# Kernel tuning notes

Hardware: AMD Instinct MI355X
Metric: run time of the kernel (lower is better)

## Reference

```python
import jax, jax.numpy as jnp
import numpy as np

PS = 2      # patch_size
TOPK = 3    # topk


def setup_inputs() -> dict:
    key = jax.random.key(0)
    x = jax.random.normal(key, (8, 128, 64, 64), dtype=jnp.float32)
    alpha = jnp.asarray(5.0, dtype=jnp.float32)  # nn.Parameter alpha
    return {"x": x, "alpha": alpha}


def _forward(x, alpha):
    ps = PS
    b, c, h, w = x.shape
    nph, npw = h // ps, w // ps
    npatch = nph * npw
    pa = ps * ps
    # F.normalize(p=2, dim=-3) with torch eps=1e-12
    norm = jnp.maximum(jnp.sqrt(jnp.sum(x * x, axis=1, keepdims=True)), 1e-12)
    x = x / norm
    # patchify -> [b, c, npatch, patch_area] (patches h-major, pixels row-major)
    xp = x.reshape(b, c, nph, ps, npw, ps).transpose(0, 1, 2, 4, 3, 5)
    xp = xp.reshape(b, c, npatch, pa)
    diag_idx = jnp.arange(ps) * (ps + 1)  # [0, 3] for ps=2
    # gather diagonal pixels of each patch -> [b, ps, npatch, c]
    xd = xp[:, :, :, diag_idx].transpose(0, 3, 2, 1)
    # patch correlation matmul -> [b, ps, npatch, npatch]
    corr = jnp.einsum('bpnc,bpmc->bpnm', xd, xd)
    avg = jnp.mean(corr, axis=1, keepdims=True)
    s = jnp.concatenate([corr, avg], axis=1)  # [b, ps+1, npatch, npatch]
    # ZeroWindow gaussian mask (rat_s=0.05); channel index = patch center (r,c)
    sr, sc = 0.05 * nph, 0.05 * npw
    rr = jnp.arange(nph, dtype=jnp.float32)
    cc = jnp.arange(npw, dtype=jnp.float32)
    cent_r, cent_c = jnp.meshgrid(rr, cc, indexing='ij')
    cent_r = cent_r.reshape(npatch)
    cent_c = cent_c.reshape(npatch)
    gr = jnp.exp(-(rr[None, :] - cent_r[:, None]) ** 2 / (2.0 * sr * sr))  # [npatch, nph]
    gc = jnp.exp(-(cc[None, :] - cent_c[:, None]) ** 2 / (2.0 * sc * sc))  # [npatch, npw]
    mask = (1.0 - gr[:, :, None] * gc[:, None, :]).reshape(npatch, npatch)
    s = s * mask[None, None]
    a = s * alpha
    # double (row + col) softmax
    s = jax.nn.softmax(a, axis=-1) * jax.nn.softmax(a, axis=-2)
    # expand avg channel to all patch pixels, scatter diagonal channels back
    new_x = jnp.broadcast_to(s[:, -1:], (b, pa, npatch, npatch))
    new_x = new_x.at[:, diag_idx].set(s[:, :ps])
    # un-patchify second npatch axis to spatial [b, npatch, h, w]
    y = jnp.swapaxes(new_x, 1, 3)  # [b, npatch, npatch, pa]
    y = y.reshape(b, npatch, nph, npw, ps, ps).transpose(0, 1, 2, 4, 3, 5)
    y = y.reshape(b, npatch, h, w)
    # topk over the npatch axis (dim=-3)
    vals = jax.lax.top_k(jnp.moveaxis(y, 1, -1), TOPK)[0]  # [b, h, w, k]
    return jnp.moveaxis(vals, -1, 1)  # [b, k, h, w]


def reference(x, alpha):
    return _forward(x, alpha)
```

## Files before the change

### kernel.cpp

```cpp
#include <hip/hip_runtime.h>
#include <hip/hip_bf16.h>
#include <math.h>

#define NB 8
#define NC 128
#define NH 64
#define NW 64
#define NP 1024
#define TWO_SIG2 5.12f
#define LOG2E 1.44269504089f
#define NT 6

static const size_t PSUM_OFF_B = 0;
static const size_t CAND_OFF_B = (size_t)NB * 3 * 4 * NP * 4;
static const size_t XD_OFF_B   = CAND_OFF_B + (size_t)NB * NP * 3 * 4 * NT * 4;

typedef __bf16 bf16x8 __attribute__((ext_vector_type(8)));
typedef float f32x4 __attribute__((ext_vector_type(4)));

#define INSERT3(v, A, Bq, Cq)                          \
  {                                                    \
    const float _na = fmaxf(A, (v));                   \
    const float _nb = __builtin_amdgcn_fmed3f(A, Bq, (v)); \
    Cq = __builtin_amdgcn_fmed3f(Bq, Cq, (v));         \
    A = _na;                                           \
    Bq = _nb;                                          \
  }

#define INSERT4(v, A, Bq, Cq, Dq)                      \
  {                                                    \
    const float _na = fmaxf(A, (v));                   \
    const float _nb = __builtin_amdgcn_fmed3f(A, Bq, (v)); \
    const float _nc = __builtin_amdgcn_fmed3f(Bq, Cq, (v)); \
    Dq = __builtin_amdgcn_fmed3f(Cq, Dq, (v));         \
    A = _na; Bq = _nb; Cq = _nc;                       \
  }

__device__ __forceinline__ float packf(float g, unsigned idx) {
  return __uint_as_float((__float_as_uint(g) & 0xFFFFFF00u) | idx);
}

__global__ __launch_bounds__(1024) void k1_norm(const float* __restrict__ x,
                                                __hip_bfloat16* __restrict__ xd) {
  __shared__ __align__(16) float tile[NC * 65];
  const int chunk = blockIdx.x;
  const int p = blockIdx.y;
  const int b = blockIdx.z;
  const int t = threadIdx.x;
  const int pix = t & 63;
  const int cw = t >> 6;
  const int nbase = chunk * 64;

  {
    const int n = nbase + pix;
    const int i = ((n >> 5) << 1) + p;
    const int jf = (n & 31);
    const float* xb = x + (size_t)b * NC * NH * NW + (size_t)i * NW;
    for (int cc = 0; cc < 8; ++cc) {
      const int c = (cc << 4) + cw;
      const float2 v2 = ((const float2*)(xb + (size_t)c * NH * NW))[jf];
      tile[c * 65 + pix] = (p == 0) ? v2.x : v2.y;
    }
  }
  __syncthreads();

  const int lane = t & 63;
  const int w = t >> 6;
  for (int pg = 0; pg < 4; ++pg) {
    const int pixel = (pg << 4) + w;
    const float v0 = tile[lane * 65 + pixel];
    const float v1 = tile[(lane + 64) * 65 + pixel];
    float ss = v0 * v0 + v1 * v1;
#pragma unroll
    for (int m = 32; m >= 1; m >>= 1) ss += __shfl_xor(ss, m, 64);
    const float inv = 1.0f / fmaxf(sqrtf(ss), 1e-12f);
    __hip_bfloat16* xr = xd + ((size_t)((b * 2 + p) * NP) + nbase + pixel) * NC;
    xr[lane] = __float2bfloat16(v0 * inv);
    xr[lane + 64] = __float2bfloat16(v1 * inv);
  }
}

__global__ __launch_bounds__(256) void k2_sums(const ushort* __restrict__ xd,
                                               const float* __restrict__ alpha_p,
                                               float* __restrict__ psum,
                                               float* __restrict__ cand) {
  __shared__ __align__(16) __bf16 Bs[2][64 * 136];
  __shared__ float stage[64][3][NT];
  const int t = threadIdx.x;
  const float K = (*alpha_p) * LOG2E;
  const float Cm = -(LOG2E / TWO_SIG2);

  const int cchunk = blockIdx.x;
  const int rowtile = blockIdx.y;
  const int b = blockIdx.z;
  const int i0 = rowtile << 6;
  const int jb = cchunk << 8;

  const int wave = t >> 6;
  const int lane = t & 63;
  const int lrow = lane & 15;
  const int kq = lane >> 4;

  const __bf16* X = (const __bf16*)xd;
  const __bf16* xp0 = X + ((size_t)(b * 2 + 0) * NP) * NC;
  const __bf16* xp1 = X + ((size_t)(b * 2 + 1) * NP) * NC;

  bf16x8 a0[4], a1[4];
  {
    const __bf16* pa0 = xp0 + (size_t)(i0 + wave * 16 + lrow) * NC + kq * 8;
    const __bf16* pa1 = xp1 + (size_t)(i0 + wave * 16 + lrow) * NC + kq * 8;
#pragma unroll
    for (int kc = 0; kc < 4; ++kc) {
      a0[kc] = *(const bf16x8*)(pa0 + kc * 32);
      a1[kc] = *(const bf16x8*)(pa1 + kc * 32);
    }
  }

  const int n0 = i0 + wave * 16 + kq * 4;
  const float rnf = (float)(n0 >> 5);
  const float cn0 = (float)(n0 & 31);

  float sums[3][4];
  float Lc[3][4][4];
#pragma unroll
  for (int ch = 0; ch < 3; ++ch)
#pragma unroll
    for (int reg = 0; reg < 4; ++reg) {
      sums[ch][reg] = 0.f;
#pragma unroll
      for (int q = 0; q < 4; ++q) Lc[ch][reg][q] = -3.0e38f;
    }

  for (int sc = 0; sc < 4; ++sc) {
    const int j0 = jb + (sc << 6);
    if (sc) __syncthreads();
#pragma unroll
    for (int pl = 0; pl < 2; ++pl) {
      const float4* gb = (const float4*)(xd + ((size_t)(b * 2 + pl) * NP + j0) * NC);
#pragma unroll
      for (int it = 0; it < 4; ++it) {
        const int f = (it << 8) + t;
        const int r = f >> 4, q = f & 15;
        *(float4*)(&Bs[pl][r * 136 + q * 8]) = gb[f];
      }
    }
    __syncthreads();

    f32x4 acc[2][4];
#pragma unroll
    for (int pl = 0; pl < 2; ++pl)
#pragma unroll
      for (int ct = 0; ct < 4; ++ct)
#pragma unroll
        for (int u = 0; u < 4; ++u) acc[pl][ct][u] = 0.f;

#pragma unroll
    for (int kc = 0; kc < 4; ++kc) {
      const int kk = kc * 32 + (kq << 3);
#pragma unroll
      for (int ct = 0; ct < 4; ++ct) {
        const bf16x8 b0 = *(const bf16x8*)(&Bs[0][(ct * 16 + lrow) * 136 + kk]);
        const bf16x8 b1 = *(const bf16x8*)(&Bs[1][(ct * 16 + lrow) * 136 + kk]);
        acc[0][ct] = __builtin_amdgcn_mfma_f32_16x16x32_bf16(a0[kc], b0, acc[0][ct], 0, 0, 0);
        acc[1][ct] = __builtin_amdgcn_mfma_f32_16x16x32_bf16(a1[kc], b1, acc[1][ct], 0, 0, 0);
      }
    }

#pragma unroll
    for (int ct = 0; ct < 4; ++ct) {
      const int mc = (sc << 6) + ct * 16 + lrow;
      const int m = jb + mc;
      const float rmf = (float)(m >> 5);
      const float cmf = (float)(m & 31);
      const float dr = rnf - rmf;
      const float dr2 = dr * dr;
      const unsigned mcu = (unsigned)mc;
#pragma unroll
      for (int reg = 0; reg < 4; ++reg) {
        const float dc = cn0 + (float)reg - cmf;
        const float d2 = fmaf(dc, dc, dr2);
        const float em = __builtin_amdgcn_exp2f(d2 * Cm);
        const float fm2 = fmaf(-em, K, K);
        const float g0 = fm2 * acc[0][ct][reg];
        const float g1 = fm2 * acc[1][ct][reg];
        sums[0][reg] += __builtin_amdgcn_exp2f(g0);
        sums[1][reg] += __builtin_amdgcn_exp2f(g1);
        sums[2][reg] += __builtin_amdgcn_exp2f(0.5f * (g0 + g1));
        const float p0 = packf(g0, mcu);
        const float p1 = packf(g1, mcu);
        const float p2 = packf(g0 + g1, mcu);
        INSERT4(p0, Lc[0][reg][0], Lc[0][reg][1], Lc[0][reg][2], Lc[0][reg][3]);
        INSERT4(p1, Lc[1][reg][0], Lc[1][reg][1], Lc[1][reg][2], Lc[1][reg][3]);
        INSERT4(p2, Lc[2][reg][0], Lc[2][reg][1], Lc[2][reg][2], Lc[2][reg][3]);
      }
    }
  }

#pragma unroll
  for (int off = 1; off < 16; off <<= 1)
#pragma unroll
    for (int ch = 0; ch < 3; ++ch)
#pragma unroll
      for (int reg = 0; reg < 4; ++reg)
        sums[ch][reg] += __shfl_xor(sums[ch][reg], off, 64);

  if (lrow == 0) {
#pragma unroll
    for (int ch = 0; ch < 3; ++ch)
#pragma unroll
      for (int reg = 0; reg < 4; ++reg) {
        const int n = i0 + wave * 16 + kq * 4 + reg;
        psum[(((size_t)b * 3 + ch) * 4 + cchunk) * NP + n] = sums[ch][reg];
      }
  }

#pragma unroll
  for (int ch = 0; ch < 3; ++ch)
#pragma unroll
    for (int reg = 0; reg < 4; ++reg) {
      float l0 = Lc[ch][reg][0], l1 = Lc[ch][reg][1];
      float l2 = Lc[ch][reg][2], l3 = Lc[ch][reg][3];
      const int np = wave * 16 + kq * 4 + reg;
#pragma unroll
      for (int r = 0; r < NT; ++r) {
        float mx = l0;
        mx = fmaxf(mx, __shfl_xor(mx, 1, 64));
        mx = fmaxf(mx, __shfl_xor(mx, 2, 64));
        mx = fmaxf(mx, __shfl_xor(mx, 4, 64));
        mx = fmaxf(mx, __shfl_xor(mx, 8, 64));
        if (lrow == 0) stage[np][ch][r] = mx;
        const bool own = (l0 == mx);
        l0 = own ? l1 : l0;
        l1 = own ? l2 : l1;
        l2 = own ? l3 : l2;
        l3 = own ? -3.0e38f : l3;
      }
    }
  __syncthreads();

  for (int u = t; u < 64 * 3 * NT; u += 256) {
    const int np = u / (3 * NT);
    const int rem = u - np * (3 * NT);
    const int ch = rem / NT;
    const int r = rem - ch * NT;
    cand[(((size_t)b * NP + i0 + np) * 3 + ch) * (4 * NT) + cchunk * NT + r] =
        stage[np][ch][r];
  }
}

__global__ __launch_bounds__(256) void k5_final(const float* __restrict__ cand,
                                                const float* __restrict__ psum,
                                                float* __restrict__ out) {
  __shared__ float nlR[3][NP];
  const int t = threadIdx.x;
  const int tau = blockIdx.x * 256 + t;
  const int b = tau >> 10;
  const int n = tau & (NP - 1);

#pragma unroll
  for (int ch = 0; ch < 3; ++ch)
#pragma unroll
    for (int k = 0; k < 4; ++k) {
      const int m = (k << 8) + t;
      const float* pp = psum + ((size_t)b * 3 + ch) * 4 * NP + m;
      nlR[ch][m] = -__builtin_amdgcn_logf(pp[0] + pp[NP] + pp[2 * NP] + pp[3 * NP]);
    }
  __syncthreads();

  float irn[3];
#pragma unroll
  for (int ch = 0; ch < 3; ++ch) {
    const float* pp = psum + ((size_t)b * 3 + ch) * 4 * NP + n;
    irn[ch] = 1.0f / (pp[0] + pp[NP] + pp[2 * NP] + pp[3 * NP]);
  }

  float o0[3], o1[3], o2[3];
#pragma unroll
  for (int ch = 0; ch < 3; ++ch) {
    float tA = -3.0e38f, tB = -3.0e38f, tC = -3.0e38f;
    const float cf = (ch == 2) ? 1.0f : 2.0f;
    const float* cp = cand + (((size_t)b * NP + n) * 3 + ch) * (4 * NT);
#pragma unroll
    for (int cc = 0; cc < 4; ++cc)
#pragma unroll
      for (int r = 0; r < NT; ++r) {
        const float p = cp[cc * NT + r];
        const int mi = (cc << 8) | (int)(__float_as_uint(p) & 255u);
        const float tv = fmaf(cf, p, nlR[ch][mi]);
        INSERT3(tv, tA, tB, tC);
      }
    o0[ch] = __builtin_amdgcn_exp2f(tA) * irn[ch];
    o1[ch] = __builtin_amdgcn_exp2f(tB) * irn[ch];
    o2[ch] = __builtin_amdgcn_exp2f(tC) * irn[ch];
  }

  const int rn = n >> 5, cn = n & 31;
  float* ob = out + (size_t)b * 3 * (NH * NW);
  const int i00 = ((rn << 1) * NW) + (cn << 1);
#pragma unroll
  for (int tt = 0; tt < 3; ++tt) {
    float* op = ob + (size_t)tt * (NH * NW);
    const float r0 = (tt == 0) ? o0[0] : (tt == 1) ? o1[0] : o2[0];
    const float r1 = (tt == 0) ? o0[1] : (tt == 1) ? o1[1] : o2[1];
    const float r2 = (tt == 0) ? o0[2] : (tt == 1) ? o1[2] : o2[2];
    op[i00] = r0;
    op[i00 + NW + 1] = r1;
    op[i00 + 1] = r2;
    op[i00 + NW] = r2;
  }
}

extern "C" void kernel_launch(void* const* d_in, const int* in_sizes, int n_in,
                              void* d_out, int out_size, void* d_ws, size_t ws_size,
                              hipStream_t stream) {
  const float* x = (const float*)d_in[0];
  const float* alpha = (const float*)d_in[1];
  float* out = (float*)d_out;
  char* ws = (char*)d_ws;

  float* psum = (float*)(ws + PSUM_OFF_B);
  float* cand = (float*)(ws + CAND_OFF_B);
  __hip_bfloat16* xd = (__hip_bfloat16*)(ws + XD_OFF_B);

  k1_norm<<<dim3(16, 2, NB), 1024, 0, stream>>>(x, xd);
  k2_sums<<<dim3(4, 16, NB), 256, 0, stream>>>((const ushort*)xd, alpha, psum, cand);
  k5_final<<<dim3(32), 256, 0, stream>>>(cand, psum, out);
}
```

Before: 103.3 us.

## Double-buffer B tiles via async global_load_lds with XOR-swizzled LDS layout

After: 114.4 us. 10.8% more time.

```diff
diff --git a/kernel.cpp b/kernel.cpp
--- a/kernel.cpp
+++ b/kernel.cpp
@@ -84,7 +84,7 @@
                                                const float* __restrict__ alpha_p,
                                                float* __restrict__ psum,
                                                float* __restrict__ cand) {
-  __shared__ __align__(16) __bf16 Bs[2][64 * 136];
+  __shared__ __align__(16) __bf16 Bs[2][2][64 * 128];
   __shared__ float stage[64][3][NT];
   const int t = threadIdx.x;
   const float K = (*alpha_p) * LOG2E;
@@ -116,6 +116,25 @@
     }
   }
 
+  const int srow_l = lane >> 4;
+  const int sslot = lane & 15;
+
+#define ISSUE_TILE(buf, j0v)                                                   \
+  {                                                                            \
+    _Pragma("unroll")                                                          \
+    for (int pl = 0; pl < 2; ++pl) {                                           \
+      const ushort* gsrc = xd + ((size_t)(b * 2 + pl) * NP + (j0v)) * NC;      \
+      _Pragma("unroll")                                                        \
+      for (int it2 = 0; it2 < 4; ++it2) {                                      \
+        const int git = wave * 4 + it2;                \
+        const int row = git * 4 + srow_l;                           \
+        const int qlog = sslot ^ (row & 7);                                    \
+        const ushort* src = gsrc + (size_t)row * NC + qlog * 8;                \
+        __builtin_amdgcn_global_load_lds(src, &Bs[buf][pl][git * 512], 16, 0, 0); \
+      }                                                                        \
+    }                                                                          \
+  }
+
   const int n0 = i0 + wave * 16 + kq * 4;
   const float rnf = (float)(n0 >> 5);
   const float cn0 = (float)(n0 & 31);
@@ -131,20 +150,15 @@
       for (int q = 0; q < 4; ++q) Lc[ch][reg][q] = -3.0e38f;
     }
 
+  ISSUE_TILE(0, jb);
+  __syncthreads();
+
+#pragma unroll
   for (int sc = 0; sc < 4; ++sc) {
+    const int cur = sc & 1;
     const int j0 = jb + (sc << 6);
-    if (sc) __syncthreads();
-#pragma unroll
-    for (int pl = 0; pl < 2; ++pl) {
-      const float4* gb = (const float4*)(xd + ((size_t)(b * 2 + pl) * NP + j0) * NC);
-#pragma unroll
-      for (int it = 0; it < 4; ++it) {
-        const int f = (it << 8) + t;
-        const int r = f >> 4, q = f & 15;
-        *(float4*)(&Bs[pl][r * 136 + q * 8]) = gb[f];
-      }
-    }
-    __syncthreads();
+
+    if (sc < 3) ISSUE_TILE(cur ^ 1, jb + ((sc + 1) << 6));
 
     f32x4 acc[2][4];
 #pragma unroll
@@ -156,11 +170,13 @@
 
 #pragma unroll
     for (int kc = 0; kc < 4; ++kc) {
-      const int kk = kc * 32 + (kq << 3);
 #pragma unroll
       for (int ct = 0; ct < 4; ++ct) {
-        const bf16x8 b0 = *(const bf16x8*)(&Bs[0][(ct * 16 + lrow) * 136 + kk]);
-        const bf16x8 b1 = *(const bf16x8*)(&Bs[1][(ct * 16 + lrow) * 136 + kk]);
+        const int row = ct * 16 + lrow;
+        const int s = kc * 4 + kq;
+        const int off = row * 128 + ((s ^ (lrow & 7)) << 3);
+        const bf16x8 b0 = *(const bf16x8*)(&Bs[cur][0][off]);
+        const bf16x8 b1 = *(const bf16x8*)(&Bs[cur][1][off]);
         acc[0][ct] = __builtin_amdgcn_mfma_f32_16x16x32_bf16(a0[kc], b0, acc[0][ct], 0, 0, 0);
         acc[1][ct] = __builtin_amdgcn_mfma_f32_16x16x32_bf16(a1[kc], b1, acc[1][ct], 0, 0, 0);
       }
@@ -194,6 +210,8 @@
         INSERT4(p2, Lc[2][reg][0], Lc[2][reg][1], Lc[2][reg][2], Lc[2][reg][3]);
       }
     }
+
+    __syncthreads();
   }
 
 #pragma unroll
@@ -246,6 +264,7 @@
     cand[(((size_t)b * NP + i0 + np) * 3 + ch) * (4 * NT) + cchunk * NT + r] =
         stage[np][ch][r];
   }
+#undef ISSUE_TILE
 }
 
 __global__ __launch_bounds__(256) void k5_final(const float* __restrict__ cand,
```

## Split k2 column tiles across two wave groups with 512-thread blocks

Applied to the files above, without the earlier changes.

New measurement: 114.1 us. +10.5%, slower.

```diff
diff --git a/kernel.cpp b/kernel.cpp
--- a/kernel.cpp
+++ b/kernel.cpp
@@ -10,10 +10,11 @@
 #define TWO_SIG2 5.12f
 #define LOG2E 1.44269504089f
 #define NT 6
+#define NHALF 8
 
 static const size_t PSUM_OFF_B = 0;
-static const size_t CAND_OFF_B = (size_t)NB * 3 * 4 * NP * 4;
-static const size_t XD_OFF_B   = CAND_OFF_B + (size_t)NB * NP * 3 * 4 * NT * 4;
+static const size_t CAND_OFF_B = (size_t)NB * 3 * NHALF * NP * 4;
+static const size_t XD_OFF_B   = CAND_OFF_B + (size_t)NB * NP * 3 * NHALF * NT * 4;
 
 typedef __bf16 bf16x8 __attribute__((ext_vector_type(8)));
 typedef float f32x4 __attribute__((ext_vector_type(4)));
@@ -80,12 +81,12 @@
   }
 }
 
-__global__ __launch_bounds__(256) void k2_sums(const ushort* __restrict__ xd,
-                                               const float* __restrict__ alpha_p,
-                                               float* __restrict__ psum,
-                                               float* __restrict__ cand) {
+__global__ __launch_bounds__(512, 4) void k2_sums(const ushort* __restrict__ xd,
+                                                  const float* __restrict__ alpha_p,
+                                                  float* __restrict__ psum,
+                                                  float* __restrict__ cand) {
   __shared__ __align__(16) __bf16 Bs[2][64 * 136];
-  __shared__ float stage[64][3][NT];
+  __shared__ float stage[64][3][2][NT];
   const int t = threadIdx.x;
   const float K = (*alpha_p) * LOG2E;
   const float Cm = -(LOG2E / TWO_SIG2);
@@ -100,6 +101,8 @@
   const int lane = t & 63;
   const int lrow = lane & 15;
   const int kq = lane >> 4;
+  const int wg = wave >> 2;
+  const int wr = wave & 3;
 
   const __bf16* X = (const __bf16*)xd;
   const __bf16* xp0 = X + ((size_t)(b * 2 + 0) * NP) * NC;
@@ -107,8 +110,8 @@
 
   bf16x8 a0[4], a1[4];
   {
-    const __bf16* pa0 = xp0 + (size_t)(i0 + wave * 16 + lrow) * NC + kq * 8;
-    const __bf16* pa1 = xp1 + (size_t)(i0 + wave * 16 + lrow) * NC + kq * 8;
+    const __bf16* pa0 = xp0 + (size_t)(i0 + wr * 16 + lrow) * NC + kq * 8;
+    const __bf16* pa1 = xp1 + (size_t)(i0 + wr * 16 + lrow) * NC + kq * 8;
 #pragma unroll
     for (int kc = 0; kc < 4; ++kc) {
       a0[kc] = *(const bf16x8*)(pa0 + kc * 32);
@@ -116,7 +119,7 @@
     }
   }
 
-  const int n0 = i0 + wave * 16 + kq * 4;
+  const int n0 = i0 + wr * 16 + kq * 4;
   const float rnf = (float)(n0 >> 5);
   const float cn0 = (float)(n0 & 31);
 
@@ -138,36 +141,38 @@
     for (int pl = 0; pl < 2; ++pl) {
       const float4* gb = (const float4*)(xd + ((size_t)(b * 2 + pl) * NP + j0) * NC);
 #pragma unroll
-      for (int it = 0; it < 4; ++it) {
-        const int f = (it << 8) + t;
+      for (int it = 0; it < 2; ++it) {
+        const int f = (it << 9) + t;
         const int r = f >> 4, q = f & 15;
         *(float4*)(&Bs[pl][r * 136 + q * 8]) = gb[f];
       }
     }
     __syncthreads();
 
-    f32x4 acc[2][4];
+    f32x4 acc[2][2];
 #pragma unroll
     for (int pl = 0; pl < 2; ++pl)
 #pragma unroll
-      for (int ct = 0; ct < 4; ++ct)
-#pragma unroll
-        for (int u = 0; u < 4; ++u) acc[pl][ct][u] = 0.f;
+      for (int cti = 0; cti < 2; ++cti)
+#pragma unroll
+        for (int u = 0; u < 4; ++u) acc[pl][cti][u] = 0.f;
 
 #pragma unroll
     for (int kc = 0; kc < 4; ++kc) {
       const int kk = kc * 32 + (kq << 3);
 #pragma unroll
-      for (int ct = 0; ct < 4; ++ct) {
+      for (int cti = 0; cti < 2; ++cti) {
+        const int ct = wg * 2 + cti;
         const bf16x8 b0 = *(const bf16x8*)(&Bs[0][(ct * 16 + lrow) * 136 + kk]);
         const bf16x8 b1 = *(const bf16x8*)(&Bs[1][(ct * 16 + lrow) * 136 + kk]);
-        acc[0][ct] = __builtin_amdgcn_mfma_f32_16x16x32_bf16(a0[kc], b0, acc[0][ct], 0, 0, 0);
-        acc[1][ct] = __builtin_amdgcn_mfma_f32_16x16x32_bf16(a1[kc], b1, acc[1][ct], 0, 0, 0);
-      }
-    }
-
-#pragma unroll
-    for (int ct = 0; ct < 4; ++ct) {
+        acc[0][cti] = __builtin_amdgcn_mfma_f32_16x16x32_bf16(a0[kc], b0, acc[0][cti], 0, 0, 0);
+        acc[1][cti] = __builtin_amdgcn_mfma_f32_16x16x32_bf16(a1[kc], b1, acc[1][cti], 0, 0, 0);
+      }
+    }
+
+#pragma unroll
+    for (int cti = 0; cti < 2; ++cti) {
+      const int ct = wg * 2 + cti;
       const int mc = (sc << 6) + ct * 16 + lrow;
       const int m = jb + mc;
       const float rmf = (float)(m >> 5);
@@ -181,8 +186,8 @@
         const float d2 = fmaf(dc, dc, dr2);
         const float em = __builtin_amdgcn_exp2f(d2 * Cm);
         const float fm2 = fmaf(-em, K, K);
-        const float g0 = fm2 * acc[0][ct][reg];
-        const float g1 = fm2 * acc[1][ct][reg];
+        const float g0 = fm2 * acc[0][cti][reg];
+        const float g1 = fm2 * acc[1][cti][reg];
         sums[0][reg] += __builtin_amdgcn_exp2f(g0);
         sums[1][reg] += __builtin_amdgcn_exp2f(g1);
         sums[2][reg] += __builtin_amdgcn_exp2f(0.5f * (g0 + g1));
@@ -209,8 +214,8 @@
     for (int ch = 0; ch < 3; ++ch)
 #pragma unroll
       for (int reg = 0; reg < 4; ++reg) {
-        const int n = i0 + wave * 16 + kq * 4 + reg;
-        psum[(((size_t)b * 3 + ch) * 4 + cchunk) * NP + n] = sums[ch][reg];
+        const int n = i0 + wr * 16 + kq * 4 + reg;
+        psum[(((size_t)b * 3 + ch) * NHALF + cchunk * 2 + wg) * NP + n] = sums[ch][reg];
       }
   }
 
@@ -220,7 +225,7 @@
     for (int reg = 0; reg < 4; ++reg) {
       float l0 = Lc[ch][reg][0], l1 = Lc[ch][reg][1];
       float l2 = Lc[ch][reg][2], l3 = Lc[ch][reg][3];
-      const int np = wave * 16 + kq * 4 + reg;
+      const int np = wr * 16 + kq * 4 + reg;
 #pragma unroll
       for (int r = 0; r < NT; ++r) {
         float mx = l0;
@@ -228,7 +233,7 @@
         mx = fmaxf(mx, __shfl_xor(mx, 2, 64));
         mx = fmaxf(mx, __shfl_xor(mx, 4, 64));
         mx = fmaxf(mx, __shfl_xor(mx, 8, 64));
-        if (lrow == 0) stage[np][ch][r] = mx;
+        if (lrow == 0) stage[np][ch][wg][r] = mx;
         const bool own = (l0 == mx);
         l0 = own ? l1 : l0;
         l1 = own ? l2 : l1;
@@ -238,13 +243,15 @@
     }
   __syncthreads();
 
-  for (int u = t; u < 64 * 3 * NT; u += 256) {
-    const int np = u / (3 * NT);
-    const int rem = u - np * (3 * NT);
-    const int ch = rem / NT;
-    const int r = rem - ch * NT;
-    cand[(((size_t)b * NP + i0 + np) * 3 + ch) * (4 * NT) + cchunk * NT + r] =
-        stage[np][ch][r];
+  for (int u = t; u < 64 * 3 * 2 * NT; u += 512) {
+    const int np = u / (3 * 2 * NT);
+    const int rem = u - np * (3 * 2 * NT);
+    const int ch = rem / (2 * NT);
+    const int rem2 = rem - ch * (2 * NT);
+    const int h = rem2 / NT;
+    const int r = rem2 - h * NT;
+    cand[((((size_t)b * NP + i0 + np) * 3 + ch) * NHALF + cchunk * 2 + h) * NT + r] =
+        stage[np][ch][h][r];
   }
 }
 
@@ -262,16 +269,22 @@
 #pragma unroll
     for (int k = 0; k < 4; ++k) {
       const int m = (k << 8) + t;
-      const float* pp = psum + ((size_t)b * 3 + ch) * 4 * NP + m;
-      nlR[ch][m] = -__builtin_amdgcn_logf(pp[0] + pp[NP] + pp[2 * NP] + pp[3 * NP]);
+      const float* pp = psum + ((size_t)b * 3 + ch) * NHALF * NP + m;
+      float s = 0.f;
+#pragma unroll
+      for (int i = 0; i < NHALF; ++i) s += pp[i * NP];
+      nlR[ch][m] = -__builtin_amdgcn_logf(s);
     }
   __syncthreads();
 
   float irn[3];
 #pragma unroll
   for (int ch = 0; ch < 3; ++ch) {
-    const float* pp = psum + ((size_t)b * 3 + ch) * 4 * NP + n;
-    irn[ch] = 1.0f / (pp[0] + pp[NP] + pp[2 * NP] + pp[3 * NP]);
+    const float* pp = psum + ((size_t)b * 3 + ch) * NHALF * NP + n;
+    float s = 0.f;
+#pragma unroll
+    for (int i = 0; i < NHALF; ++i) s += pp[i * NP];
+    irn[ch] = 1.0f / s;
   }
 
   float o0[3], o1[3], o2[3];
@@ -279,13 +292,13 @@
   for (int ch = 0; ch < 3; ++ch) {
     float tA = -3.0e38f, tB = -3.0e38f, tC = -3.0e38f;
     const float cf = (ch == 2) ? 1.0f : 2.0f;
-    const float* cp = cand + (((size_t)b * NP + n) * 3 + ch) * (4 * NT);
-#pragma unroll
-    for (int cc = 0; cc < 4; ++cc)
+    const float* cp = cand + (((size_t)b * NP + n) * 3 + ch) * (NHALF * NT);
+#pragma unroll
+    for (int h = 0; h < NHALF; ++h)
 #pragma unroll
       for (int r = 0; r < NT; ++r) {
-        const float p = cp[cc * NT + r];
-        const int mi = (cc << 8) | (int)(__float_as_uint(p) & 255u);
+        const float p = cp[h * NT + r];
+        const int mi = ((h >> 1) << 8) | (int)(__float_as_uint(p) & 255u);
         const float tv = fmaf(cf, p, nlR[ch][mi]);
         INSERT3(tv, tA, tB, tC);
       }
@@ -323,6 +336,6 @@
   __hip_bfloat16* xd = (__hip_bfloat16*)(ws + XD_OFF_B);
 
   k1_norm<<<dim3(16, 2, NB), 1024, 0, stream>>>(x, xd);
-  k2_sums<<<dim3(4, 16, NB), 256, 0, stream>>>((const ushort*)xd, alpha, psum, cand);
+  k2_sums<<<dim3(4, 16, NB), 512, 0, stream>>>((const ushort*)xd, alpha, psum, cand);
   k5_final<<<dim3(32), 256, 0, stream>>>(cand, psum, out);
 }
```
